# Kernel optimization log

Measured on AMD Instinct MI355X. Metric: run time of the kernel, lower is better.

## Reference

```python
import jax, jax.numpy as jnp
import numpy as np

MARGIN = 1.0


def setup_inputs() -> dict:
    key = jax.random.key(0)
    k1, k2, k3 = jax.random.split(key, 3)
    B, P = 8192, 16
    return {
        "energies": jax.random.normal(k1, (B, 1), dtype=jnp.float32),
        "property_values": jax.random.normal(k2, (B, P), dtype=jnp.float32),
        "property_targets": jax.random.normal(k3, (P,), dtype=jnp.float32),
    }


def reference(energies, property_values, property_targets):
    # distances[i] = ||property_values[i] - property_targets||_2, shape [B]
    distances = jnp.linalg.norm(property_values - property_targets[None, :], axis=-1)
    B = energies.shape[0]
    e = energies[:, 0]  # [B]
    # pair mask: i != j and distances[i] < distances[j]  -> [B, B]
    mask = (distances[:, None] < distances[None, :]) & (~jnp.eye(B, dtype=bool))
    # ranking loss per pair: relu(e_i - e_j + margin)
    pair_loss = jax.nn.relu(e[:, None] - e[None, :] + MARGIN)
    loss_sum = jnp.sum(jnp.where(mask, pair_loss, 0.0))
    count = jnp.sum(mask).astype(jnp.float32)
    loss = loss_sum / jnp.maximum(count, 1.0)
    # torch version accumulates [1]-shaped tensors -> output shape [1]
    return loss[None]
```

## Files before the change

### kernel.cpp

```cpp
#include <hip/hip_runtime.h>
#include <math.h>

#define MARGIN 1.0f
#define NI 16
#define BMAX 8192

struct Ctl {
    double sacc;
    double cacc;
    unsigned ticket;
    unsigned pad;
};

__global__ __launch_bounds__(256) void dist_init_kernel(
    const float* __restrict__ pv,
    const float* __restrict__ pt,
    float* __restrict__ dist,
    Ctl* __restrict__ ctl,
    int B, int P)
{
    int i = blockIdx.x * 256 + threadIdx.x;
    if (i == 0) { ctl->sacc = 0.0; ctl->cacc = 0.0; ctl->ticket = 0u; }
    if (i >= B) return;
    const float* row = pv + (size_t)i * P;
    float s = 0.f;
    if (P == 16) {
        const float4* r4 = (const float4*)row;
        const float4* t4 = (const float4*)pt;
        #pragma unroll
        for (int q = 0; q < 4; ++q) {
            float4 r = r4[q], t = t4[q];
            float d0 = r.x - t.x; s = fmaf(d0, d0, s);
            float d1 = r.y - t.y; s = fmaf(d1, d1, s);
            float d2 = r.z - t.z; s = fmaf(d2, d2, s);
            float d3 = r.w - t.w; s = fmaf(d3, d3, s);
        }
    } else {
        for (int p = 0; p < P; ++p) { float d = row[p] - pt[p]; s = fmaf(d, d, s); }
    }
    dist[i] = sqrtf(s);
}

__global__ __launch_bounds__(256) void pair_fused_kernel(
    const float* __restrict__ e,
    const float* __restrict__ dist,
    Ctl* __restrict__ ctl,
    float* __restrict__ out,
    int B, int nblocks)
{
    __shared__ float sd[BMAX];
    __shared__ float se[BMAX];
    const int tid = threadIdx.x;

    {
        const int n4 = B >> 2;
        const float4* d4 = (const float4*)dist;
        const float4* e4 = (const float4*)e;
        float4* sd4 = (float4*)sd;
        float4* se4 = (float4*)se;
        for (int k = tid; k < n4; k += 256) { sd4[k] = d4[k]; se4[k] = e4[k]; }
        for (int k = (n4 << 2) + tid; k < B; k += 256) { sd[k] = dist[k]; se[k] = e[k]; }
        for (int k = B + tid; k < BMAX; k += 256) { sd[k] = -INFINITY; se[k] = 0.f; }
    }
    __syncthreads();

    const int i0 = blockIdx.x * NI;
    float di[NI], ai[NI];
    #pragma unroll
    for (int ii = 0; ii < NI; ++ii) {
        const bool iok = (i0 + ii) < B;
        di[ii] = iok ? sd[i0 + ii] : INFINITY;
        ai[ii] = iok ? (se[i0 + ii] + MARGIN) : 0.f;
    }

    float s0 = 0.f, s1 = 0.f, s2 = 0.f, s3 = 0.f;
    unsigned c0 = 0u, c1 = 0u, c2 = 0u, c3 = 0u;

    for (int s = 0; s < (BMAX / 256); ++s) {
        const int j = (s << 8) + tid;
        const float dj = sd[j];
        const float ej = se[j];
        #pragma unroll
        for (int ii = 0; ii < NI; ii += 4) {
            { const bool m = di[ii]   < dj; const float t = fmaxf(ai[ii]   - ej, 0.f); s0 += m ? t : 0.f; c0 += (unsigned)m; }
            { const bool m = di[ii+1] < dj; const float t = fmaxf(ai[ii+1] - ej, 0.f); s1 += m ? t : 0.f; c1 += (unsigned)m; }
            { const bool m = di[ii+2] < dj; const float t = fmaxf(ai[ii+2] - ej, 0.f); s2 += m ? t : 0.f; c2 += (unsigned)m; }
            { const bool m = di[ii+3] < dj; const float t = fmaxf(ai[ii+3] - ej, 0.f); s3 += m ? t : 0.f; c3 += (unsigned)m; }
        }
    }

    float sum = (s0 + s1) + (s2 + s3);
    float cnt = (float)((c0 + c1) + (c2 + c3));
    #pragma unroll
    for (int o = 32; o > 0; o >>= 1) {
        sum += __shfl_xor(sum, o);
        cnt += __shfl_xor(cnt, o);
    }

    __syncthreads();
    const int wid = tid >> 6;
    if ((tid & 63) == 0) { sd[wid] = sum; se[wid] = cnt; }
    __syncthreads();

    if (tid == 0) {
        double S = ((double)sd[0] + (double)sd[1]) + ((double)sd[2] + (double)sd[3]);
        double C = ((double)se[0] + (double)se[1]) + ((double)se[2] + (double)se[3]);
        atomicAdd(&ctl->sacc, S);
        atomicAdd(&ctl->cacc, C);
        __threadfence();
        unsigned t = atomicAdd(&ctl->ticket, 1u);
        if (t == (unsigned)(nblocks - 1)) {
            double fs = atomicAdd(&ctl->sacc, 0.0);
            double fc = atomicAdd(&ctl->cacc, 0.0);
            if (fc < 1.0) fc = 1.0;
            out[0] = (float)(fs / fc);
        }
    }
}

extern "C" void kernel_launch(void* const* d_in, const int* in_sizes, int n_in,
                              void* d_out, int out_size, void* d_ws, size_t ws_size,
                              hipStream_t stream)
{
    const float* energies = (const float*)d_in[0];
    const float* pv       = (const float*)d_in[1];
    const float* pt       = (const float*)d_in[2];
    int B = in_sizes[0];
    int P = in_sizes[2];

    float* dist = (float*)d_ws;
    size_t coff = (((size_t)BMAX * sizeof(float)) + 255) & ~(size_t)255;
    Ctl* ctl = (Ctl*)((char*)d_ws + coff);

    int nblocks = (B + NI - 1) / NI;

    dist_init_kernel<<<(B + 255) / 256, 256, 0, stream>>>(pv, pt, dist, ctl, B, P);
    pair_fused_kernel<<<nblocks, 256, 0, stream>>>(energies, dist, ctl, (float*)d_out, B, nblocks);
}
```

Baseline: 88.39 us.

## Stream pair data from global memory instead of staging whole arrays in LDS

The pair kernel no longer copies the full distance and energy arrays (64 KB) into shared memory. Each thread now streams them straight from global memory as float4 with a one-step register prefetch. The atomic/ticket cross-block reduction is replaced by per-block partial writes plus a separate single-block finalize kernel. This removes the per-block LDS fill and its occupancy limit, at the cost of a third launch and global/L2 reads for every j element.

Result: faster. 71.17 us (-19.5%).

```diff
diff --git a/kernel.cpp b/kernel.cpp
--- a/kernel.cpp
+++ b/kernel.cpp
@@ -3,24 +3,14 @@
 
 #define MARGIN 1.0f
 #define NI 16
-#define BMAX 8192
 
-struct Ctl {
-    double sacc;
-    double cacc;
-    unsigned ticket;
-    unsigned pad;
-};
-
-__global__ __launch_bounds__(256) void dist_init_kernel(
+__global__ __launch_bounds__(256) void dist_kernel(
     const float* __restrict__ pv,
     const float* __restrict__ pt,
     float* __restrict__ dist,
-    Ctl* __restrict__ ctl,
     int B, int P)
 {
     int i = blockIdx.x * 256 + threadIdx.x;
-    if (i == 0) { ctl->sacc = 0.0; ctl->cacc = 0.0; ctl->ticket = 0u; }
     if (i >= B) return;
     const float* row = pv + (size_t)i * P;
     float s = 0.f;
@@ -41,45 +31,29 @@
     dist[i] = sqrtf(s);
 }
 
-__global__ __launch_bounds__(256) void pair_fused_kernel(
+__global__ __launch_bounds__(256) void pair_kernel(
     const float* __restrict__ e,
     const float* __restrict__ dist,
-    Ctl* __restrict__ ctl,
-    float* __restrict__ out,
-    int B, int nblocks)
+    float* __restrict__ psum,
+    float* __restrict__ pcnt,
+    int B)
 {
-    __shared__ float sd[BMAX];
-    __shared__ float se[BMAX];
     const int tid = threadIdx.x;
+    const int i0 = blockIdx.x * NI;
 
-    {
-        const int n4 = B >> 2;
-        const float4* d4 = (const float4*)dist;
-        const float4* e4 = (const float4*)e;
-        float4* sd4 = (float4*)sd;
-        float4* se4 = (float4*)se;
-        for (int k = tid; k < n4; k += 256) { sd4[k] = d4[k]; se4[k] = e4[k]; }
-        for (int k = (n4 << 2) + tid; k < B; k += 256) { sd[k] = dist[k]; se[k] = e[k]; }
-        for (int k = B + tid; k < BMAX; k += 256) { sd[k] = -INFINITY; se[k] = 0.f; }
-    }
-    __syncthreads();
-
-    const int i0 = blockIdx.x * NI;
     float di[NI], ai[NI];
     #pragma unroll
     for (int ii = 0; ii < NI; ++ii) {
-        const bool iok = (i0 + ii) < B;
-        di[ii] = iok ? sd[i0 + ii] : INFINITY;
-        ai[ii] = iok ? (se[i0 + ii] + MARGIN) : 0.f;
+        const int i = i0 + ii;
+        const bool iok = i < B;
+        di[ii] = iok ? dist[i] : INFINITY;
+        ai[ii] = iok ? (e[i] + MARGIN) : 0.f;
     }
 
     float s0 = 0.f, s1 = 0.f, s2 = 0.f, s3 = 0.f;
     unsigned c0 = 0u, c1 = 0u, c2 = 0u, c3 = 0u;
 
-    for (int s = 0; s < (BMAX / 256); ++s) {
-        const int j = (s << 8) + tid;
-        const float dj = sd[j];
-        const float ej = se[j];
+    auto proc = [&](float dj, float ej) {
         #pragma unroll
         for (int ii = 0; ii < NI; ii += 4) {
             { const bool m = di[ii]   < dj; const float t = fmaxf(ai[ii]   - ej, 0.f); s0 += m ? t : 0.f; c0 += (unsigned)m; }
@@ -87,6 +61,32 @@
             { const bool m = di[ii+2] < dj; const float t = fmaxf(ai[ii+2] - ej, 0.f); s2 += m ? t : 0.f; c2 += (unsigned)m; }
             { const bool m = di[ii+3] < dj; const float t = fmaxf(ai[ii+3] - ej, 0.f); s3 += m ? t : 0.f; c3 += (unsigned)m; }
         }
+    };
+
+    const int nvec = B >> 2;
+    const float4* d4 = (const float4*)dist;
+    const float4* e4 = (const float4*)e;
+
+    const int nfull = nvec >> 8;
+    float4 dc, ec;
+    if (nfull > 0) { dc = d4[tid]; ec = e4[tid]; }
+    for (int s = 0; s < nfull; ++s) {
+        float4 dn, en;
+        const bool more = (s + 1) < nfull;
+        const int jn = ((s + 1) << 8) + tid;
+        if (more) { dn = d4[jn]; en = e4[jn]; }
+        proc(dc.x, ec.x);
+        proc(dc.y, ec.y);
+        proc(dc.z, ec.z);
+        proc(dc.w, ec.w);
+        if (more) { dc = dn; ec = en; }
+    }
+    for (int j4 = (nfull << 8) + tid; j4 < nvec; j4 += 256) {
+        const float4 dv = d4[j4], ev = e4[j4];
+        proc(dv.x, ev.x); proc(dv.y, ev.y); proc(dv.z, ev.z); proc(dv.w, ev.w);
+    }
+    for (int j = (nvec << 2) + tid; j < B; j += 256) {
+        proc(dist[j], e[j]);
     }
 
     float sum = (s0 + s1) + (s2 + s3);
@@ -97,24 +97,42 @@
         cnt += __shfl_xor(cnt, o);
     }
 
+    __shared__ float rs[4], rc[4];
+    const int wid = tid >> 6;
+    if ((tid & 63) == 0) { rs[wid] = sum; rc[wid] = cnt; }
     __syncthreads();
-    const int wid = tid >> 6;
-    if ((tid & 63) == 0) { sd[wid] = sum; se[wid] = cnt; }
+    if (tid == 0) {
+        psum[blockIdx.x] = (rs[0] + rs[1]) + (rs[2] + rs[3]);
+        pcnt[blockIdx.x] = (rc[0] + rc[1]) + (rc[2] + rc[3]);
+    }
+}
+
+__global__ __launch_bounds__(256) void finalize_kernel(
+    const float* __restrict__ psum,
+    const float* __restrict__ pcnt,
+    float* __restrict__ out,
+    int nblk)
+{
+    __shared__ double ss[256];
+    __shared__ double sc[256];
+    double s = 0.0, c = 0.0;
+    for (int k = threadIdx.x; k < nblk; k += 256) {
+        s += (double)psum[k];
+        c += (double)pcnt[k];
+    }
+    ss[threadIdx.x] = s;
+    sc[threadIdx.x] = c;
     __syncthreads();
-
-    if (tid == 0) {
-        double S = ((double)sd[0] + (double)sd[1]) + ((double)sd[2] + (double)sd[3]);
-        double C = ((double)se[0] + (double)se[1]) + ((double)se[2] + (double)se[3]);
-        atomicAdd(&ctl->sacc, S);
-        atomicAdd(&ctl->cacc, C);
-        __threadfence();
-        unsigned t = atomicAdd(&ctl->ticket, 1u);
-        if (t == (unsigned)(nblocks - 1)) {
-            double fs = atomicAdd(&ctl->sacc, 0.0);
-            double fc = atomicAdd(&ctl->cacc, 0.0);
-            if (fc < 1.0) fc = 1.0;
-            out[0] = (float)(fs / fc);
+    for (int st = 128; st > 0; st >>= 1) {
+        if ((int)threadIdx.x < st) {
+            ss[threadIdx.x] += ss[threadIdx.x + st];
+            sc[threadIdx.x] += sc[threadIdx.x + st];
         }
+        __syncthreads();
+    }
+    if (threadIdx.x == 0) {
+        double cnt = sc[0] < 1.0 ? 1.0 : sc[0];
+        out[0] = (float)(ss[0] / cnt);
     }
 }
 
@@ -128,12 +146,13 @@
     int B = in_sizes[0];
     int P = in_sizes[2];
 
+    int nblk = (B + NI - 1) / NI;
+
     float* dist = (float*)d_ws;
-    size_t coff = (((size_t)BMAX * sizeof(float)) + 255) & ~(size_t)255;
-    Ctl* ctl = (Ctl*)((char*)d_ws + coff);
+    float* psum = dist + B;
+    float* pcnt = psum + nblk;
 
-    int nblocks = (B + NI - 1) / NI;
-
-    dist_init_kernel<<<(B + 255) / 256, 256, 0, stream>>>(pv, pt, dist, ctl, B, P);
-    pair_fused_kernel<<<nblocks, 256, 0, stream>>>(energies, dist, ctl, (float*)d_out, B, nblocks);
+    dist_kernel<<<(B + 255) / 256, 256, 0, stream>>>(pv, pt, dist, B, P);
+    pair_kernel<<<nblk, 256, 0, stream>>>(energies, dist, psum, pcnt, B);
+    finalize_kernel<<<1, 256, 0, stream>>>(psum, pcnt, (float*)d_out, nblk);
 }
```
